# Performance work log

Measured on AMD Instinct MI355X. Metric: run time of the kernel, lower is better.

## Reference

```python
import jax, jax.numpy as jnp
import numpy as np
from jax import lax

TAGSET_SIZE = 50
K = TAGSET_SIZE + 2          # +START, +STOP
START_TAG = TAGSET_SIZE      # 50
STOP_TAG = TAGSET_SIZE + 1   # 51
B, T = 1024, 512
NEG_INF = -10000.0


def setup_inputs() -> dict:
    key = jax.random.key(0)
    k1, k2, k3, k4 = jax.random.split(key, 4)
    logits = jax.random.normal(k1, (B, T, K), dtype=jnp.float32)
    transitions = jax.random.normal(k2, (K, K), dtype=jnp.float32)
    labels = jax.random.randint(k3, (B, T), 0, TAGSET_SIZE)          # real tags only
    lens = jax.random.randint(k4, (B,), 1, T + 1)                    # at least 1 token
    return {"logits": logits, "transitions": transitions, "labels": labels, "lens": lens}


def _crf_nll(logits, transitions, labels, lens):
    b, t, k = logits.shape

    # ---- forward algorithm (log partition) ----
    alpha0 = jnp.full((b, k), NEG_INF, dtype=logits.dtype).at[:, START_TAG].set(0.0)
    step_mask = jnp.arange(t)[None, :] < lens[:, None]               # [B,T] True while c_lens > 0

    def step(alpha, inp):
        logit_t, m_t = inp                                           # [B,K], [B]
        # alpha_nxt[b,i] = logsumexp_j(trans[i,j] + alpha[b,j]) + logit[b,i]
        mat = alpha[:, None, :] + transitions[None, :, :]            # [B,K,K]
        alpha_nxt = jax.nn.logsumexp(mat, axis=2) + logit_t
        alpha = jnp.where(m_t[:, None], alpha_nxt, alpha)
        return alpha, None

    alpha, _ = lax.scan(step, alpha0, (jnp.swapaxes(logits, 0, 1), step_mask.T))
    alpha = alpha + transitions[STOP_TAG][None, :]
    partition = jax.nn.logsumexp(alpha, axis=1)                      # [B]

    # ---- transition score of gold path ----
    start_col = jnp.full((b, 1), START_TAG, dtype=labels.dtype)
    stop_col = jnp.full((b, 1), STOP_TAG, dtype=labels.dtype)
    labels_ext = jnp.concatenate([start_col, labels, stop_col], axis=1)  # [B,T+2]
    pos = jnp.arange(t + 2)[None, :]
    keep = pos < (lens + 1)[:, None]                                 # positions <= lens keep tag, rest -> STOP
    labels_ext = jnp.where(keep, labels_ext, STOP_TAG)
    prev, nxt = labels_ext[:, :-1], labels_ext[:, 1:]                # [B,T+1]
    trn_scr = transitions[nxt, prev]                                 # trans[next, prev]
    m_trn = (jnp.arange(t + 1)[None, :] < (lens + 1)[:, None]).astype(logits.dtype)
    transition_score = jnp.sum(trn_scr * m_trn, axis=1)              # [B]

    # ---- emission score of gold path ----
    em = jnp.take_along_axis(logits, labels[:, :, None], axis=2)[:, :, 0]  # [B,T]
    m_em = (jnp.arange(t)[None, :] < lens[:, None]).astype(logits.dtype)
    emission_score = jnp.sum(em * m_em, axis=1)                      # [B]

    # faithful to source: partition + emission - transition
    return partition + emission_score - transition_score


def reference(logits, transitions, labels, lens):
    return _crf_nll(logits, transitions, labels, lens)
```

## Files before the change

kernel.cpp:

```cpp
#include <hip/hip_runtime.h>

#define KTAG 52
#define START_TAG 50
#define STOP_TAG 51
#define TMAX 512
#define NCU 256

__device__ __forceinline__ float rdlanef(float v, int l) {
    return __int_as_float(__builtin_amdgcn_readlane(__float_as_int(v), l));
}

__device__ __forceinline__ float matv(const float* __restrict__ Erow, float v) {
    float a0 = 0.f, a1 = 0.f, a2 = 0.f, a3 = 0.f;
    #pragma unroll
    for (int j = 0; j < 13; ++j) {
        a0 = fmaf(Erow[4*j+0], rdlanef(v, 4*j+0), a0);
        a1 = fmaf(Erow[4*j+1], rdlanef(v, 4*j+1), a1);
        a2 = fmaf(Erow[4*j+2], rdlanef(v, 4*j+2), a2);
        a3 = fmaf(Erow[4*j+3], rdlanef(v, 4*j+3), a3);
    }
    return (a0 + a1) + (a2 + a3);
}

template<bool BWD>
__device__ __forceinline__ float chain(const float* __restrict__ p0, int stride,
                                       int maxk, int nsteps, const float* __restrict__ Erow,
                                       float beta, float& M2) {
    constexpr float L2E = 1.4426950408889634f;
    M2 = 0.f;

    auto lgt = [&](int k) -> float {
        int kc = k < maxk ? k : maxk;
        return p0[(long)stride * kc];
    };
    auto STEP = [&](float lg, float scl) {
        float e = exp2f(lg * L2E);
        if (BWD) beta = matv(Erow, beta * e * scl);
        else     beta = matv(Erow, beta * scl) * e;
    };

    float l0 = lgt(0), l1 = lgt(1), l2 = lgt(2), l3 = lgt(3);
    int k = 0;
    while (k + 4 <= nsteps) {
        float n0 = lgt(k+4), n1 = lgt(k+5), n2 = lgt(k+6), n3 = lgt(k+7);
        float scl = 1.f;
        if (k > 0) {
            float m = fmaxf(rdlanef(beta, 0), 1e-30f);
            M2 += log2f(m);
            scl = 1.f / m;
        }
        STEP(l0, scl); STEP(l1, 1.f); STEP(l2, 1.f); STEP(l3, 1.f);
        l0 = n0; l1 = n1; l2 = n2; l3 = n3;
        k += 4;
    }
    if (k < nsteps) {
        float scl = 1.f;
        if (k > 0) {
            float m = fmaxf(rdlanef(beta, 0), 1e-30f);
            M2 += log2f(m);
            scl = 1.f / m;
        }
        STEP(l0, scl); ++k;
        if (k < nsteps) { STEP(l1, 1.f); ++k; }
        if (k < nsteps) { STEP(l2, 1.f); ++k; }
    }
    return beta;
}

#define LPL 16
__global__ __launch_bounds__(64) void rank_kernel(
    const int* __restrict__ lens, int* __restrict__ perm, int B)
{
    const int lane = threadIdx.x;
    int myl[LPL];
    #pragma unroll
    for (int k = 0; k < LPL; ++k) {
        int j = lane * LPL + k;
        myl[k] = (j < B) ? lens[j] : 0x7fffffff;
    }
    const int base = blockIdx.x * 64;
    for (int i = 0; i < 64; ++i) {
        int b = base + i;
        if (b >= B) break;
        int Lb = lens[b];
        int r = 0;
        #pragma unroll
        for (int k = 0; k < LPL; ++k) {
            int j = lane * LPL + k;
            r += (myl[k] < Lb || (myl[k] == Lb && j < b)) ? 1 : 0;
        }
        #pragma unroll
        for (int off = 32; off; off >>= 1) r += __shfl_xor(r, off);
        if (lane == 0) perm[r] = b;
    }
}

__global__ __launch_bounds__(128, 1) void crf_split_kernel(
    const float* __restrict__ logits,
    const float* __restrict__ trans,
    const int*   __restrict__ labels,
    const int*   __restrict__ lens,
    const int*   __restrict__ perm,
    float* __restrict__ out, int B)
{
    constexpr float L2E = 1.4426950408889634f;
    constexpr float LN2 = 0.6931471805599453f;

    const int blk  = blockIdx.x;
    const int wave = threadIdx.x >> 6;
    const int lane = threadIdx.x & 63;
    const bool active = lane < KTAG;
    const bool bwd = (wave == 1);

    int r = blk;
    if (B == 4 * NCU) {
        int m = blk & (NCU - 1), j = blk >> 8;
        r = (j == 0) ? m
          : (j == 1) ? (2 * NCU - 1 - m)
          : (j == 2) ? (2 * NCU + m)
          :            (4 * NCU - 1 - m);
    }
    const int batch = perm[r];
    const int len = lens[batch];
    const int mid = len >> 1;

    float Erow[KTAG];
    #pragma unroll
    for (int j = 0; j < KTAG; ++j) {
        float tv = active ? (bwd ? trans[j * KTAG + lane]
                                 : trans[(size_t)lane * KTAG + j]) : 0.f;
        Erow[j] = active ? exp2f(tv * L2E) : 0.f;
    }

    const float* base = logits + (size_t)batch * TMAX * KTAG + (active ? lane : 0);

    __shared__ __align__(16) float sB[64];
    __shared__ float sM2f, sEm, sTr;

    float M2, beta;
    if (bwd) {
        float b0 = active ? exp2f(trans[STOP_TAG * KTAG + lane] * L2E) : 0.f;
        beta = chain<true>(base + (size_t)(len - 1) * KTAG, -KTAG,
                           len - 1, len - mid, Erow, b0, M2);
    } else {
        float b0 = (lane == START_TAG) ? 1.f : 0.f;
        beta = chain<false>(base, KTAG, TMAX - 1, mid, Erow, b0, M2);

        const int*   labp = labels + (size_t)batch * TMAX;
        const float* lgb  = logits + (size_t)batch * TMAX * KTAG;
        int lab[8], prv[8]; bool msk[8];
        #pragma unroll
        for (int c = 0; c < 8; ++c) {
            int tt = c * 64 + lane;
            msk[c] = tt < len;
            int ttc = msk[c] ? tt : 0;
            lab[c] = labp[ttc];
            prv[c] = (ttc == 0) ? START_TAG : labp[ttc - 1];
        }
        float em = 0.f, tr = 0.f;
        #pragma unroll
        for (int c = 0; c < 8; ++c) {
            int ttc = msk[c] ? (c * 64 + lane) : 0;
            float ev = lgb[(size_t)ttc * KTAG + lab[c]];
            float tv = trans[lab[c] * KTAG + prv[c]];
            if (msk[c]) { em += ev; tr += tv; }
        }
        if (lane == 0) tr += trans[STOP_TAG * KTAG + labp[len - 1]];
        #pragma unroll
        for (int off = 32; off; off >>= 1) {
            em += __shfl_xor(em, off);
            tr += __shfl_xor(tr, off);
        }
        sB[lane] = beta;
        if (lane == 0) { sM2f = M2; sEm = em; sTr = tr; }
    }
    __syncthreads();

    if (bwd) {
        float d = beta * sB[lane];
        #pragma unroll
        for (int off = 32; off; off >>= 1) d += __shfl_xor(d, off);
        float partition = LN2 * (sM2f + M2 + log2f(d));
        if (lane == 0) out[batch] = partition + sEm - sTr;
    }
}

extern "C" void kernel_launch(void* const* d_in, const int* in_sizes, int n_in,
                              void* d_out, int out_size, void* d_ws, size_t ws_size,
                              hipStream_t stream) {
    const float* logits = (const float*)d_in[0];
    const float* trans  = (const float*)d_in[1];
    const int*   labels = (const int*)d_in[2];
    const int*   lens   = (const int*)d_in[3];
    float* out = (float*)d_out;

    const int B = in_sizes[3];
    int* perm = (int*)d_ws;

    rank_kernel<<<dim3((B + 63) / 64), dim3(64), 0, stream>>>(lens, perm, B);
    crf_split_kernel<<<dim3(B), dim3(128), 0, stream>>>(
        logits, trans, labels, lens, perm, out, B);
}
```

Baseline: 127.4 us.

## Pipeline readlanes in matvec, shuffle lens in rank kernel, remap block-to-rank order

```diff
diff --git a/kernel.cpp b/kernel.cpp
--- a/kernel.cpp
+++ b/kernel.cpp
@@ -10,15 +10,24 @@
     return __int_as_float(__builtin_amdgcn_readlane(__float_as_int(v), l));
 }
 
-__device__ __forceinline__ float matv(const float* __restrict__ Erow, float v) {
+__device__ __forceinline__ float matv(const float* __restrict__ E, float x) {
     float a0 = 0.f, a1 = 0.f, a2 = 0.f, a3 = 0.f;
+    float s0 = rdlanef(x, 0), s1 = rdlanef(x, 1),
+          s2 = rdlanef(x, 2), s3 = rdlanef(x, 3);
     #pragma unroll
-    for (int j = 0; j < 13; ++j) {
-        a0 = fmaf(Erow[4*j+0], rdlanef(v, 4*j+0), a0);
-        a1 = fmaf(Erow[4*j+1], rdlanef(v, 4*j+1), a1);
-        a2 = fmaf(Erow[4*j+2], rdlanef(v, 4*j+2), a2);
-        a3 = fmaf(Erow[4*j+3], rdlanef(v, 4*j+3), a3);
-    }
+    for (int j = 0; j < 48; j += 4) {
+        float t0 = rdlanef(x, j + 4), t1 = rdlanef(x, j + 5),
+              t2 = rdlanef(x, j + 6), t3 = rdlanef(x, j + 7);
+        a0 = fmaf(E[j + 0], s0, a0);
+        a1 = fmaf(E[j + 1], s1, a1);
+        a2 = fmaf(E[j + 2], s2, a2);
+        a3 = fmaf(E[j + 3], s3, a3);
+        s0 = t0; s1 = t1; s2 = t2; s3 = t3;
+    }
+    a0 = fmaf(E[48], s0, a0);
+    a1 = fmaf(E[49], s1, a1);
+    a2 = fmaf(E[50], s2, a2);
+    a3 = fmaf(E[51], s3, a3);
     return (a0 + a1) + (a2 + a3);
 }
 
@@ -79,10 +88,11 @@
         myl[k] = (j < B) ? lens[j] : 0x7fffffff;
     }
     const int base = blockIdx.x * 64;
+    const int Lme = (base + lane < B) ? lens[base + lane] : 0x7fffffff;
     for (int i = 0; i < 64; ++i) {
         int b = base + i;
         if (b >= B) break;
-        int Lb = lens[b];
+        int Lb = __shfl(Lme, i);
         int r = 0;
         #pragma unroll
         for (int k = 0; k < LPL; ++k) {
@@ -114,11 +124,8 @@
 
     int r = blk;
     if (B == 4 * NCU) {
-        int m = blk & (NCU - 1), j = blk >> 8;
-        r = (j == 0) ? m
-          : (j == 1) ? (2 * NCU - 1 - m)
-          : (j == 2) ? (2 * NCU + m)
-          :            (4 * NCU - 1 - m);
+        int q = blk & (NCU - 1), j = blk >> 8;
+        r = 4 * q + j;
     }
     const int batch = perm[r];
     const int len = lens[batch];
```

New measurement: 145.5 us. 14.2% more time.
